# Kernel optimization log

Hardware: AMD Instinct MI355X
Metric: run time of the kernel (lower is better)

Reference implementation:

```python
import jax, jax.numpy as jnp
import numpy as np

DOWNSAMPLE = 512  # points per cloud, from init_kwargs


def _pairwise_dist(x, y):
    """Batched Euclidean distance matrix. x: (B,n,D), y: (B,m,D) -> (B,n,m)."""
    x2 = jnp.sum(x * x, axis=-1)                     # (B,n)
    y2 = jnp.sum(y * y, axis=-1)                     # (B,m)
    d2 = x2[:, :, None] + y2[:, None, :] - 2.0 * jnp.einsum('bnd,bmd->bnm', x, y)
    pos = d2 > 0.0                                   # guard sqrt(0)/negatives from fp error
    return jnp.where(pos, jnp.sqrt(jnp.where(pos, d2, 1.0)), 0.0)


def setup_inputs() -> dict:
    key = jax.random.key(0)
    k1, k2 = jax.random.split(key)
    inp = jax.random.normal(k1, (65536, 128), dtype=jnp.float32)
    tgt = jax.random.normal(k2, (65536, 128), dtype=jnp.float32)
    return {"input": inp, "target": tgt}


def reference(input, target):
    D = input.shape[-1]
    x = input.reshape(-1, DOWNSAMPLE, D)   # (B, n, D)
    y = target.reshape(-1, DOWNSAMPLE, D)  # (B, n, D)
    # geomloss energy kernel loss with uniform weights:
    # L_b = mean||x-y|| - 0.5*mean||x-x'|| - 0.5*mean||y-y'||
    cross = jnp.mean(_pairwise_dist(x, y), axis=(1, 2))  # (B,)
    xx = jnp.mean(_pairwise_dist(x, x), axis=(1, 2))
    yy = jnp.mean(_pairwise_dist(y, y), axis=(1, 2))
    loss = cross - 0.5 * xx - 0.5 * yy
    return jnp.mean(loss)
```

## Files before the change

### kernel.cpp

```cpp
#include <hip/hip_runtime.h>

typedef __attribute__((ext_vector_type(8))) __bf16 bf16x8;
typedef __attribute__((ext_vector_type(4))) float f32x4;
typedef __attribute__((ext_vector_type(8))) unsigned short ushort8;

#define DSAMP 512
#define DIM   128
#define S1    ((size_t)16777216)
#define REG5  16384
#define NBPB  36
#define NPAIR 18
#define NORM_OFF (2 * S1)
#define PART_OFF (2 * S1 + 524288)
#define WS_NEEDED (PART_OFF + (size_t)128 * NBPB * 4)

__global__ __launch_bounds__(256)
void presplit7(const float* __restrict__ x, const float* __restrict__ y,
               char* __restrict__ ws) {
    const int bid = blockIdx.x;
    const int xcd = bid & 7;
    const int q   = bid >> 3;
    const int bi  = q >> 6;
    const int rem = q & 63;
    const int input = rem >> 5;
    const int rg  = rem & 31;
    const int b   = xcd + 8 * bi;

    const int tid = threadIdx.x;
    const int jb  = tid & 7;
    const int c   = (tid >> 3) & 1;
    const int rb  = rg * 16 + (tid >> 4);
    const int ri  = b * 512 + rb;

    const float* src = (input ? y : x) + ((size_t)ri << 7) + c * 64 + jb * 8;
    float4 v0 = ((const float4*)src)[0];
    float4 v1 = ((const float4*)src)[1];

    float s = v0.x * v0.x + v0.y * v0.y + v0.z * v0.z + v0.w * v0.w
            + v1.x * v1.x + v1.y * v1.y + v1.z * v1.z + v1.w * v1.w;
    #pragma unroll
    for (int o = 8; o > 0; o >>= 1) s += __shfl_down(s, o, 16);

    float xs[8] = {v0.x, v0.y, v0.z, v0.w, v1.x, v1.y, v1.z, v1.w};
    ushort8 hv;
    #pragma unroll
    for (int e = 0; e < 8; ++e) {
        unsigned ub = __float_as_uint(xs[e]);
        hv[e] = (unsigned short)((ub + 0x7fffu + ((ub >> 16) & 1u)) >> 16);
    }

    char* hi = ws + (size_t)input * S1;
    size_t off = ((size_t)(b * 2 + c) * 512 + rb) * 128
               + (size_t)((jb ^ (rb & 7)) * 16);
    *(ushort8*)(hi + off) = hv;

    if ((tid & 15) == 0) {
        float* nG = (float*)(ws + NORM_OFF) + (size_t)input * 65536;
        nG[ri] = s;
    }
}

__constant__ unsigned char T_Asrc[NPAIR]  = {0,0,0,0,0,0,0,0, 1,1,1,1,1,1,1,1,1,1};
__constant__ unsigned char T_Ai[NPAIR]    = {0,0,1,1,1,2,2,3, 0,0,0,0,1,1,1,2,2,3};
__constant__ unsigned char T_Bsrc0[NPAIR] = {0,0,0,0,1,0,1,0, 1,1,0,0,1,1,0,1,0,1};
__constant__ unsigned char T_Bsrc1[NPAIR] = {0,0,0,1,1,0,1,1, 1,1,0,0,1,0,0,1,0,0};
__constant__ unsigned char T_Bj0[NPAIR]   = {0,2,1,3,2,2,2,3, 0,2,0,2,1,3,2,2,0,3};
__constant__ unsigned char T_Bj1[NPAIR]   = {1,3,2,1,3,3,3,3, 1,3,1,3,2,0,3,3,3,0};
__constant__ char          T_wc0[NPAIR]   = {2,1,2,1,0,2,0,2, 2,1,0,0,2,1,0,2,0,2};
__constant__ char          T_wc1[NPAIR]   = {1,1,1,0,0,1,0,0, 1,1,0,0,1,0,0,1,0,0};
__constant__ unsigned char T_d0[NPAIR]    = {1,0,1,0,0,1,0,1, 1,0,0,0,1,0,0,1,0,1};

__global__ __launch_bounds__(256, 3)
void mmd_pair(const char* __restrict__ ws, float* __restrict__ partials) {
    __shared__ __align__(16) char smem[3 * REG5];
    __shared__ float Pn[128];
    __shared__ float Qn0[128];
    __shared__ float Qn1[128];
    __shared__ float wred[4];

    const int tid  = threadIdx.x;
    const int bid  = blockIdx.x;
    const int xcd  = bid & 7;
    const int seq  = bid >> 3;
    const int s    = seq % NPAIR;
    const int bseq = seq / NPAIR;
    const int b    = xcd + 8 * (15 - bseq);

    const float* normX = (const float*)(ws + NORM_OFF);
    const float* normY = normX + 65536;

    const int Ai  = T_Ai[s];
    const int Bj0 = T_Bj0[s];
    const int Bj1 = T_Bj1[s];
    const char* Ap  = ws + (T_Asrc[s]  ? S1 : 0);
    const char* Bp0 = ws + (T_Bsrc0[s] ? S1 : 0);
    const char* Bp1 = ws + (T_Bsrc1[s] ? S1 : 0);
    const float* nA  = T_Asrc[s]  ? normY : normX;
    const float* nB0 = T_Bsrc0[s] ? normY : normX;
    const float* nB1 = T_Bsrc1[s] ? normY : normX;
    const int wc0 = T_wc0[s], wc1 = T_wc1[s];
    const float w0 = (wc0 == 0) ? 1.0f : ((wc0 == 1) ? -1.0f : -0.5f);
    const float w1 = (wc1 == 0) ? 1.0f : ((wc1 == 1) ? -1.0f : -0.5f);
    const bool dg0 = T_d0[s] != 0;

    if (tid < 128) {
        Pn[tid] = nA[(size_t)b * 512 + Ai * 128 + tid];
    } else {
        int qn = tid - 128;
        Qn0[qn] = nB0[(size_t)b * 512 + Bj0 * 128 + qn];
        Qn1[qn] = nB1[(size_t)b * 512 + Bj1 * 128 + qn];
    }

    const int lane    = tid & 63;
    const int wv      = tid >> 6;
    const int rowHalf = (wv >> 1) * 64;
    const int colHalf = (wv & 1) * 64;
    const int fm      = lane & 15;
    const int kq      = lane >> 4;
    const int sw      = fm & 7;

    const size_t ch0 = (size_t)(b * 2 + 0) * 512;
    const size_t ch1 = (size_t)(b * 2 + 1) * 512;

    {
        const char* sA0 = Ap  + (ch0 + (size_t)Ai  * 128) * 128;
        const char* sA1 = Ap  + (ch1 + (size_t)Ai  * 128) * 128;
        const char* sB  = Bp0 + (ch0 + (size_t)Bj0 * 128) * 128;
        #pragma unroll
        for (int f = 0; f < 12; ++f) {
            int g = wv * 12 + f;
            const char* base = (g < 16) ? sA0 : ((g < 32) ? sA1 : sB);
            const char* gs = base + (g & 15) * 1024 + lane * 16;
            char* ls = smem + (size_t)g * 1024 + lane * 16;
            __builtin_amdgcn_global_load_lds(
                (const __attribute__((address_space(1))) void*)gs,
                (__attribute__((address_space(3))) void*)ls, 16, 0, 0);
        }
    }

    auto stageB = [&](const char* Bp, int Bj, size_t ch) {
        const char* src = Bp + (ch + (size_t)Bj * 128) * 128;
        #pragma unroll
        for (int f = 0; f < 4; ++f) {
            int g = wv * 4 + f;
            const char* gs = src + g * 1024 + lane * 16;
            char* ls = smem + 2 * REG5 + (size_t)g * 1024 + lane * 16;
            __builtin_amdgcn_global_load_lds(
                (const __attribute__((address_space(1))) void*)gs,
                (__attribute__((address_space(3))) void*)ls, 16, 0, 0);
        }
    };

    f32x4 acc[4][4];
    auto zero_acc = [&]() {
        #pragma unroll
        for (int a2 = 0; a2 < 4; ++a2)
            #pragma unroll
            for (int b2 = 0; b2 < 4; ++b2)
                acc[a2][b2] = (f32x4){0.f, 0.f, 0.f, 0.f};
    };

    auto compute = [&](int creg) {
        const char* Ab = smem + creg * REG5;
        const char* Bb = smem + 2 * REG5;
        #pragma unroll
        for (int ks = 0; ks < 2; ++ks) {
            const int jx = ((ks * 4 + kq) ^ sw) * 16;
            bf16x8 ah[4], bh[4];
            #pragma unroll
            for (int a2 = 0; a2 < 4; ++a2)
                ah[a2] = *(const bf16x8*)(Ab + (rowHalf + a2 * 16 + fm) * 128 + jx);
            #pragma unroll
            for (int b2 = 0; b2 < 4; ++b2)
                bh[b2] = *(const bf16x8*)(Bb + (colHalf + b2 * 16 + fm) * 128 + jx);
            #pragma unroll
            for (int a2 = 0; a2 < 4; ++a2)
                #pragma unroll
                for (int b2 = 0; b2 < 4; ++b2)
                    acc[a2][b2] = __builtin_amdgcn_mfma_f32_16x16x32_bf16(
                        ah[a2], bh[b2], acc[a2][b2], 0, 0, 0);
        }
    };

    auto tile_sum = [&](const float* Qn, bool dg) -> float {
        float Pr[16], Qc[4];
        #pragma unroll
        for (int a2 = 0; a2 < 4; ++a2)
            #pragma unroll
            for (int rg2 = 0; rg2 < 4; ++rg2)
                Pr[a2 * 4 + rg2] = Pn[rowHalf + a2 * 16 + kq * 4 + rg2];
        #pragma unroll
        for (int b2 = 0; b2 < 4; ++b2) Qc[b2] = Qn[colHalf + b2 * 16 + fm];
        float ls = 0.f;
        if (dg) {
            #pragma unroll
            for (int a2 = 0; a2 < 4; ++a2)
                #pragma unroll
                for (int b2 = 0; b2 < 4; ++b2)
                    #pragma unroll
                    for (int rg2 = 0; rg2 < 4; ++rg2) {
                        float d2 = fmaf(-2.0f, acc[a2][b2][rg2], Pr[a2 * 4 + rg2] + Qc[b2]);
                        float v  = __builtin_amdgcn_sqrtf(fmaxf(d2, 0.0f));
                        if ((rowHalf + a2 * 16 + kq * 4 + rg2) == (colHalf + b2 * 16 + fm)) v = 0.f;
                        ls += v;
                    }
        } else {
            #pragma unroll
            for (int a2 = 0; a2 < 4; ++a2)
                #pragma unroll
                for (int b2 = 0; b2 < 4; ++b2)
                    #pragma unroll
                    for (int rg2 = 0; rg2 < 4; ++rg2) {
                        float d2 = fmaf(-2.0f, acc[a2][b2][rg2], Pr[a2 * 4 + rg2] + Qc[b2]);
                        ls += __builtin_amdgcn_sqrtf(fmaxf(d2, 0.0f));
                    }
        }
        return ls;
    };

    zero_acc();
    __syncthreads();
    compute(0);
    __syncthreads();
    stageB(Bp0, Bj0, ch1);
    __syncthreads();
    compute(1);
    __syncthreads();
    stageB(Bp1, Bj1, ch0);
    float lsum = w0 * tile_sum(Qn0, dg0);
    __syncthreads();

    zero_acc();
    compute(0);
    __syncthreads();
    stageB(Bp1, Bj1, ch1);
    __syncthreads();
    compute(1);
    lsum += w1 * tile_sum(Qn1, false);

    #pragma unroll
    for (int off = 32; off > 0; off >>= 1) lsum += __shfl_down(lsum, off, 64);
    if (lane == 0) wred[wv] = lsum;
    __syncthreads();
    if (tid == 0)
        partials[bid] = wred[0] + wred[1] + wred[2] + wred[3];
}

__global__ __launch_bounds__(256, 2)
void mmd_tile_fallback(const float* __restrict__ x, const float* __restrict__ y,
                       float* __restrict__ partials) {
    __shared__ __align__(16) char smem[4 * 128 * 144];
    __shared__ float Pn[128];
    __shared__ float Qn[128];
    __shared__ float wred[4];

    char* Ah = smem;
    char* Al = smem + 1 * 128 * 144;
    char* Bh = smem + 2 * 128 * 144;
    char* Bl = smem + 3 * 128 * 144;

    const int tid  = threadIdx.x;
    const int bid  = blockIdx.x;
    const int tj   = bid & 3;
    const int ti   = (bid >> 2) & 3;
    const int type = (bid >> 4) % 3;
    const int b    = bid / 48;

    const float* Xb = x + (size_t)b * DSAMP * DIM;
    const float* Yb = y + (size_t)b * DSAMP * DIM;
    const float* Pp; const float* Qp; float w;
    if (type == 0)      { Pp = Xb; Qp = Yb; w = 1.0f;  }
    else if (type == 1) { Pp = Xb; Qp = Xb; w = -0.5f; }
    else                { Pp = Yb; Qp = Yb; w = -0.5f; }
    Pp += (size_t)ti * 128 * DIM;
    Qp += (size_t)tj * 128 * DIM;

    {
        const float* rp = (tid < 128) ? (Pp + (size_t)tid * DIM)
                                      : (Qp + (size_t)(tid - 128) * DIM);
        float s = 0.f;
        #pragma unroll
        for (int k4 = 0; k4 < 32; ++k4) {
            float4 v = ((const float4*)rp)[k4];
            s += v.x * v.x + v.y * v.y + v.z * v.z + v.w * v.w;
        }
        if (tid < 128) Pn[tid] = s; else Qn[tid - 128] = s;
    }

    const int lane    = tid & 63;
    const int wv      = tid >> 6;
    const int rowHalf = (wv >> 1) * 64;
    const int colHalf = (wv & 1) * 64;
    const int fm      = lane & 15;
    const int kq      = lane >> 4;

    f32x4 acc[4][4];
    #pragma unroll
    for (int a2 = 0; a2 < 4; ++a2)
        #pragma unroll
        for (int b2 = 0; b2 < 4; ++b2)
            acc[a2][b2] = (f32x4){0.f, 0.f, 0.f, 0.f};

    for (int c = 0; c < 2; ++c) {
        if (c) __syncthreads();
        #pragma unroll
        for (int side = 0; side < 2; ++side) {
            const float* sp = side ? Qp : Pp;
            char* dh = side ? Bh : Ah;
            char* dl = side ? Bl : Al;
            #pragma unroll
            for (int it = 0; it < 4; ++it) {
                int u  = it * 256 + tid;
                int r  = u >> 3;
                int c8 = u & 7;
                const float* g = sp + (size_t)r * DIM + c * 64 + c8 * 8;
                float4 v0 = ((const float4*)g)[0];
                float4 v1 = ((const float4*)g)[1];
                float xs[8] = {v0.x, v0.y, v0.z, v0.w, v1.x, v1.y, v1.z, v1.w};
                ushort8 hv, lv;
                #pragma unroll
                for (int e = 0; e < 8; ++e) {
                    float xv = xs[e];
                    unsigned ub = __float_as_uint(xv);
                    unsigned hr = (ub + 0x7fffu + ((ub >> 16) & 1u)) >> 16;
                    float hf = __uint_as_float(hr << 16);
                    float rs = xv - hf;
                    unsigned ul = __float_as_uint(rs);
                    unsigned lr = (ul + 0x7fffu + ((ul >> 16) & 1u)) >> 16;
                    hv[e] = (unsigned short)hr;
                    lv[e] = (unsigned short)lr;
                }
                *(ushort8*)(dh + r * 144 + c8 * 16) = hv;
                *(ushort8*)(dl + r * 144 + c8 * 16) = lv;
            }
        }
        __syncthreads();
        #pragma unroll
        for (int ks = 0; ks < 2; ++ks) {
            const int kb2 = (ks * 32 + kq * 8) * 2;
            bf16x8 ah[4], al[4], bh[4], bl[4];
            #pragma unroll
            for (int a2 = 0; a2 < 4; ++a2) {
                int ar = rowHalf + a2 * 16 + fm;
                ah[a2] = *(const bf16x8*)(Ah + ar * 144 + kb2);
                al[a2] = *(const bf16x8*)(Al + ar * 144 + kb2);
            }
            #pragma unroll
            for (int b2 = 0; b2 < 4; ++b2) {
                int br = colHalf + b2 * 16 + fm;
                bh[b2] = *(const bf16x8*)(Bh + br * 144 + kb2);
                bl[b2] = *(const bf16x8*)(Bl + br * 144 + kb2);
            }
            #pragma unroll
            for (int a2 = 0; a2 < 4; ++a2)
                #pragma unroll
                for (int b2 = 0; b2 < 4; ++b2) {
                    acc[a2][b2] = __builtin_amdgcn_mfma_f32_16x16x32_bf16(ah[a2], bh[b2], acc[a2][b2], 0, 0, 0);
                    acc[a2][b2] = __builtin_amdgcn_mfma_f32_16x16x32_bf16(ah[a2], bl[b2], acc[a2][b2], 0, 0, 0);
                    acc[a2][b2] = __builtin_amdgcn_mfma_f32_16x16x32_bf16(al[a2], bh[b2], acc[a2][b2], 0, 0, 0);
                }
        }
    }

    const bool selfm = (type != 0) && (ti == tj);
    float lsum = 0.f;
    #pragma unroll
    for (int a2 = 0; a2 < 4; ++a2) {
        int ib = rowHalf + a2 * 16 + kq * 4;
        #pragma unroll
        for (int b2 = 0; b2 < 4; ++b2) {
            int j = colHalf + b2 * 16 + fm;
            float qn = Qn[j];
            #pragma unroll
            for (int rg = 0; rg < 4; ++rg) {
                int i = ib + rg;
                float d2 = Pn[i] + qn - 2.0f * acc[a2][b2][rg];
                if (d2 > 0.f && !(selfm && i == j)) lsum += sqrtf(d2);
            }
        }
    }
    #pragma unroll
    for (int off = 32; off > 0; off >>= 1) lsum += __shfl_down(lsum, off, 64);
    if (lane == 0) wred[wv] = lsum;
    __syncthreads();
    if (tid == 0)
        partials[bid] = (wred[0] + wred[1] + wred[2] + wred[3]) * w;
}

__global__ __launch_bounds__(256)
void mmd_finalize_kernel(const float* __restrict__ partials, int n,
                         float* __restrict__ out, double scale) {
    __shared__ double sh[256];
    double s = 0.0;
    for (int i = threadIdx.x; i < n; i += 256) s += (double)partials[i];
    sh[threadIdx.x] = s;
    __syncthreads();
    for (int off = 128; off > 0; off >>= 1) {
        if ((int)threadIdx.x < off) sh[threadIdx.x] += sh[threadIdx.x + off];
        __syncthreads();
    }
    if (threadIdx.x == 0) out[0] = (float)(sh[0] * scale);
}

extern "C" void kernel_launch(void* const* d_in, const int* in_sizes, int n_in,
                              void* d_out, int out_size, void* d_ws, size_t ws_size,
                              hipStream_t stream) {
    const float* x = (const float*)d_in[0];
    const float* y = (const float*)d_in[1];
    float* out = (float*)d_out;

    const int n = in_sizes[0];
    const int B = n / (DSAMP * DIM);
    const double scale = 1.0 / ((double)B * (double)DSAMP * (double)DSAMP);

    if (ws_size >= WS_NEEDED && B == 128) {
        char* ws = (char*)d_ws;
        float* partials = (float*)(ws + PART_OFF);
        const int nblocks = B * NPAIR;
        presplit7<<<dim3(8192), dim3(256), 0, stream>>>(x, y, ws);
        mmd_pair<<<dim3(nblocks), dim3(256), 0, stream>>>(ws, partials);
        mmd_finalize_kernel<<<dim3(1), dim3(256), 0, stream>>>(partials, nblocks, out, scale);
    } else {
        float* partials = (float*)d_ws;
        const int nblocks = B * 48;
        mmd_tile_fallback<<<dim3(nblocks), dim3(256), 0, stream>>>(x, y, partials);
        mmd_finalize_kernel<<<dim3(1), dim3(256), 0, stream>>>(partials, nblocks, out, scale);
    }
}
```

Baseline: 128.3 us.

## Fuse bf16 presplit into pair kernel with register-prefetched fp32 loads

Removes the separate presplit kernel that converted inputs to swizzled bf16 and computed row norms in workspace. The pair kernel now reads the fp32 inputs directly, converts them to bf16 in registers, writes them to LDS and computes norms in place. The next B tile is prefetched into registers while the MFMA loop runs, and MFMA issue priority is raised with s_setprio. This saves a kernel launch and a round trip through workspace, but each block now reads twice the bytes (fp32), does redundant conversion across the 18 pair blocks per batch, and uses more registers.

```diff
diff --git a/kernel.cpp b/kernel.cpp
--- a/kernel.cpp
+++ b/kernel.cpp
@@ -6,59 +6,8 @@
 
 #define DSAMP 512
 #define DIM   128
-#define S1    ((size_t)16777216)
 #define REG5  16384
-#define NBPB  36
 #define NPAIR 18
-#define NORM_OFF (2 * S1)
-#define PART_OFF (2 * S1 + 524288)
-#define WS_NEEDED (PART_OFF + (size_t)128 * NBPB * 4)
-
-__global__ __launch_bounds__(256)
-void presplit7(const float* __restrict__ x, const float* __restrict__ y,
-               char* __restrict__ ws) {
-    const int bid = blockIdx.x;
-    const int xcd = bid & 7;
-    const int q   = bid >> 3;
-    const int bi  = q >> 6;
-    const int rem = q & 63;
-    const int input = rem >> 5;
-    const int rg  = rem & 31;
-    const int b   = xcd + 8 * bi;
-
-    const int tid = threadIdx.x;
-    const int jb  = tid & 7;
-    const int c   = (tid >> 3) & 1;
-    const int rb  = rg * 16 + (tid >> 4);
-    const int ri  = b * 512 + rb;
-
-    const float* src = (input ? y : x) + ((size_t)ri << 7) + c * 64 + jb * 8;
-    float4 v0 = ((const float4*)src)[0];
-    float4 v1 = ((const float4*)src)[1];
-
-    float s = v0.x * v0.x + v0.y * v0.y + v0.z * v0.z + v0.w * v0.w
-            + v1.x * v1.x + v1.y * v1.y + v1.z * v1.z + v1.w * v1.w;
-    #pragma unroll
-    for (int o = 8; o > 0; o >>= 1) s += __shfl_down(s, o, 16);
-
-    float xs[8] = {v0.x, v0.y, v0.z, v0.w, v1.x, v1.y, v1.z, v1.w};
-    ushort8 hv;
-    #pragma unroll
-    for (int e = 0; e < 8; ++e) {
-        unsigned ub = __float_as_uint(xs[e]);
-        hv[e] = (unsigned short)((ub + 0x7fffu + ((ub >> 16) & 1u)) >> 16);
-    }
-
-    char* hi = ws + (size_t)input * S1;
-    size_t off = ((size_t)(b * 2 + c) * 512 + rb) * 128
-               + (size_t)((jb ^ (rb & 7)) * 16);
-    *(ushort8*)(hi + off) = hv;
-
-    if ((tid & 15) == 0) {
-        float* nG = (float*)(ws + NORM_OFF) + (size_t)input * 65536;
-        nG[ri] = s;
-    }
-}
 
 __constant__ unsigned char T_Asrc[NPAIR]  = {0,0,0,0,0,0,0,0, 1,1,1,1,1,1,1,1,1,1};
 __constant__ unsigned char T_Ai[NPAIR]    = {0,0,1,1,1,2,2,3, 0,0,0,0,1,1,1,2,2,3};
@@ -71,45 +20,37 @@
 __constant__ unsigned char T_d0[NPAIR]    = {1,0,1,0,0,1,0,1, 1,0,0,0,1,0,0,1,0,1};
 
 __global__ __launch_bounds__(256, 3)
-void mmd_pair(const char* __restrict__ ws, float* __restrict__ partials) {
+void mmd_fused(const float* __restrict__ x, const float* __restrict__ y,
+               float* __restrict__ partials) {
     __shared__ __align__(16) char smem[3 * REG5];
     __shared__ float Pn[128];
     __shared__ float Qn0[128];
     __shared__ float Qn1[128];
     __shared__ float wred[4];
 
-    const int tid  = threadIdx.x;
-    const int bid  = blockIdx.x;
-    const int xcd  = bid & 7;
-    const int seq  = bid >> 3;
-    const int s    = seq % NPAIR;
-    const int bseq = seq / NPAIR;
-    const int b    = xcd + 8 * (15 - bseq);
-
-    const float* normX = (const float*)(ws + NORM_OFF);
-    const float* normY = normX + 65536;
+    const int tid = threadIdx.x;
+    const int bid = blockIdx.x;
+    const int xcd = bid & 7;
+    const int seq = bid >> 3;
+    const int s   = seq % NPAIR;
+    const int grp = seq / NPAIR;
+    const int b   = xcd + 8 * grp;
 
     const int Ai  = T_Ai[s];
     const int Bj0 = T_Bj0[s];
     const int Bj1 = T_Bj1[s];
-    const char* Ap  = ws + (T_Asrc[s]  ? S1 : 0);
-    const char* Bp0 = ws + (T_Bsrc0[s] ? S1 : 0);
-    const char* Bp1 = ws + (T_Bsrc1[s] ? S1 : 0);
-    const float* nA  = T_Asrc[s]  ? normY : normX;
-    const float* nB0 = T_Bsrc0[s] ? normY : normX;
-    const float* nB1 = T_Bsrc1[s] ? normY : normX;
+    const float* Asrc  = T_Asrc[s]  ? y : x;
+    const float* B0src = T_Bsrc0[s] ? y : x;
+    const float* B1src = T_Bsrc1[s] ? y : x;
     const int wc0 = T_wc0[s], wc1 = T_wc1[s];
     const float w0 = (wc0 == 0) ? 1.0f : ((wc0 == 1) ? -1.0f : -0.5f);
     const float w1 = (wc1 == 0) ? 1.0f : ((wc1 == 1) ? -1.0f : -0.5f);
     const bool dg0 = T_d0[s] != 0;
 
-    if (tid < 128) {
-        Pn[tid] = nA[(size_t)b * 512 + Ai * 128 + tid];
-    } else {
-        int qn = tid - 128;
-        Qn0[qn] = nB0[(size_t)b * 512 + Bj0 * 128 + qn];
-        Qn1[qn] = nB1[(size_t)b * 512 + Bj1 * 128 + qn];
-    }
+    const size_t rowbase = (size_t)b * 512;
+    const float* Ap  = Asrc  + (rowbase + (size_t)Ai  * 128) * 128;
+    const float* Bp0 = B0src + (rowbase + (size_t)Bj0 * 128) * 128;
+    const float* Bp1 = B1src + (rowbase + (size_t)Bj1 * 128) * 128;
 
     const int lane    = tid & 63;
     const int wv      = tid >> 6;
@@ -119,35 +60,42 @@
     const int kq      = lane >> 4;
     const int sw      = fm & 7;
 
-    const size_t ch0 = (size_t)(b * 2 + 0) * 512;
-    const size_t ch1 = (size_t)(b * 2 + 1) * 512;
-
-    {
-        const char* sA0 = Ap  + (ch0 + (size_t)Ai  * 128) * 128;
-        const char* sA1 = Ap  + (ch1 + (size_t)Ai  * 128) * 128;
-        const char* sB  = Bp0 + (ch0 + (size_t)Bj0 * 128) * 128;
-        #pragma unroll
-        for (int f = 0; f < 12; ++f) {
-            int g = wv * 12 + f;
-            const char* base = (g < 16) ? sA0 : ((g < 32) ? sA1 : sB);
-            const char* gs = base + (g & 15) * 1024 + lane * 16;
-            char* ls = smem + (size_t)g * 1024 + lane * 16;
-            __builtin_amdgcn_global_load_lds(
-                (const __attribute__((address_space(1))) void*)gs,
-                (__attribute__((address_space(3))) void*)ls, 16, 0, 0);
-        }
-    }
-
-    auto stageB = [&](const char* Bp, int Bj, size_t ch) {
-        const char* src = Bp + (ch + (size_t)Bj * 128) * 128;
-        #pragma unroll
-        for (int f = 0; f < 4; ++f) {
-            int g = wv * 4 + f;
-            const char* gs = src + g * 1024 + lane * 16;
-            char* ls = smem + 2 * REG5 + (size_t)g * 1024 + lane * 16;
-            __builtin_amdgcn_global_load_lds(
-                (const __attribute__((address_space(1))) void*)gs,
-                (__attribute__((address_space(3))) void*)ls, 16, 0, 0);
+    auto cvt_write16 = [&](float4 v0, float4 v1, char* dst) -> float {
+        float xs[8] = {v0.x, v0.y, v0.z, v0.w, v1.x, v1.y, v1.z, v1.w};
+        ushort8 hv;
+        float ss = 0.f;
+        #pragma unroll
+        for (int e = 0; e < 8; ++e) {
+            ss += xs[e] * xs[e];
+            unsigned ub = __float_as_uint(xs[e]);
+            hv[e] = (unsigned short)((ub + 0x7fffu + ((ub >> 16) & 1u)) >> 16);
+        }
+        *(ushort8*)dst = hv;
+        return ss;
+    };
+
+    auto loadB = [&](const float* Bp, int cc, float4 (*vb)[2]) {
+        #pragma unroll
+        for (int it = 0; it < 4; ++it) {
+            int u  = it * 256 + tid;
+            int jb = u & 7;
+            int r  = u >> 3;
+            const float* g = Bp + (size_t)r * 128 + cc * 64 + jb * 8;
+            vb[it][0] = ((const float4*)g)[0];
+            vb[it][1] = ((const float4*)g)[1];
+        }
+    };
+    auto writeB = [&](float4 (*vb)[2], float* Qn, bool add) {
+        #pragma unroll
+        for (int it = 0; it < 4; ++it) {
+            int u  = it * 256 + tid;
+            int jb = u & 7;
+            int r  = u >> 3;
+            float ss = cvt_write16(vb[it][0], vb[it][1],
+                                   smem + 2 * REG5 + r * 128 + ((jb ^ (r & 7)) * 16));
+            #pragma unroll
+            for (int o = 4; o > 0; o >>= 1) ss += __shfl_down(ss, o, 8);
+            if ((tid & 7) == 0) { if (add) Qn[r] += ss; else Qn[r] = ss; }
         }
     };
 
@@ -173,12 +121,14 @@
             #pragma unroll
             for (int b2 = 0; b2 < 4; ++b2)
                 bh[b2] = *(const bf16x8*)(Bb + (colHalf + b2 * 16 + fm) * 128 + jx);
+            __builtin_amdgcn_s_setprio(1);
             #pragma unroll
             for (int a2 = 0; a2 < 4; ++a2)
                 #pragma unroll
                 for (int b2 = 0; b2 < 4; ++b2)
                     acc[a2][b2] = __builtin_amdgcn_mfma_f32_16x16x32_bf16(
                         ah[a2], bh[b2], acc[a2][b2], 0, 0, 0);
+            __builtin_amdgcn_s_setprio(0);
         }
     };
 
@@ -218,22 +168,57 @@
         return ls;
     };
 
+    {
+        float4 va[8][2];
+        #pragma unroll
+        for (int it = 0; it < 8; ++it) {
+            int u  = it * 256 + tid;
+            int jb = u & 7;
+            int cc = (u >> 3) & 1;
+            int r  = u >> 4;
+            const float* g = Ap + (size_t)r * 128 + cc * 64 + jb * 8;
+            va[it][0] = ((const float4*)g)[0];
+            va[it][1] = ((const float4*)g)[1];
+        }
+        float4 vb0[4][2];
+        loadB(Bp0, 0, vb0);
+        #pragma unroll
+        for (int it = 0; it < 8; ++it) {
+            int u  = it * 256 + tid;
+            int jb = u & 7;
+            int cc = (u >> 3) & 1;
+            int r  = u >> 4;
+            float ss = cvt_write16(va[it][0], va[it][1],
+                                   smem + cc * REG5 + r * 128 + ((jb ^ (r & 7)) * 16));
+            #pragma unroll
+            for (int o = 8; o > 0; o >>= 1) ss += __shfl_down(ss, o, 16);
+            if ((tid & 15) == 0) Pn[r] = ss;
+        }
+        writeB(vb0, Qn0, false);
+    }
+    __syncthreads();
+
     zero_acc();
-    __syncthreads();
+    float4 vb1[4][2];
+    loadB(Bp0, 1, vb1);
     compute(0);
     __syncthreads();
-    stageB(Bp0, Bj0, ch1);
-    __syncthreads();
+    writeB(vb1, Qn0, true);
+    __syncthreads();
+    float4 vb2[4][2];
+    loadB(Bp1, 0, vb2);
     compute(1);
-    __syncthreads();
-    stageB(Bp1, Bj1, ch0);
     float lsum = w0 * tile_sum(Qn0, dg0);
-    __syncthreads();
-
     zero_acc();
+    __syncthreads();
+    writeB(vb2, Qn1, false);
+    __syncthreads();
+
+    float4 vb3[4][2];
+    loadB(Bp1, 1, vb3);
     compute(0);
     __syncthreads();
-    stageB(Bp1, Bj1, ch1);
+    writeB(vb3, Qn1, true);
     __syncthreads();
     compute(1);
     lsum += w1 * tile_sum(Qn1, false);
@@ -413,15 +398,12 @@
     const int B = n / (DSAMP * DIM);
     const double scale = 1.0 / ((double)B * (double)DSAMP * (double)DSAMP);
 
-    if (ws_size >= WS_NEEDED && B == 128) {
-        char* ws = (char*)d_ws;
-        float* partials = (float*)(ws + PART_OFF);
-        const int nblocks = B * NPAIR;
-        presplit7<<<dim3(8192), dim3(256), 0, stream>>>(x, y, ws);
-        mmd_pair<<<dim3(nblocks), dim3(256), 0, stream>>>(ws, partials);
+    float* partials = (float*)d_ws;
+    if (B == 128 && ws_size >= (size_t)(128 * NPAIR) * 4) {
+        const int nblocks = 128 * NPAIR;
+        mmd_fused<<<dim3(nblocks), dim3(256), 0, stream>>>(x, y, partials);
         mmd_finalize_kernel<<<dim3(1), dim3(256), 0, stream>>>(partials, nblocks, out, scale);
     } else {
-        float* partials = (float*)d_ws;
         const int nblocks = B * 48;
         mmd_tile_fallback<<<dim3(nblocks), dim3(256), 0, stream>>>(x, y, partials);
         mmd_finalize_kernel<<<dim3(1), dim3(256), 0, stream>>>(partials, nblocks, out, scale);
```

Result: slower. 182.8 us (+42.5%).
